# Performance work log

Measured on AMD Instinct MI355X. Metric: run time of the kernel, lower is better.

Reference implementation:

```python
import jax, jax.numpy as jnp
import numpy as np

B = 4096       # batch_size
D = 128        # projection dim
TEMP = 0.5     # temperature
EPS = 1e-12    # F.normalize eps


def setup_inputs() -> dict:
    key = jax.random.key(0)
    k1, k2 = jax.random.split(key)
    zi = jax.random.normal(k1, (B, D), dtype=jnp.float32)
    zj = jax.random.normal(k2, (B, D), dtype=jnp.float32)
    return {"zi": zi, "zj": zj}


def _l2_normalize(x):
    n = jnp.sqrt(jnp.sum(x * x, axis=-1, keepdims=True))
    return x / jnp.maximum(n, EPS)


def reference(zi, zj):
    zi_n = _l2_normalize(zi)
    zj_n = _l2_normalize(zj)

    # four [B, B] similarity matrices
    lii = jnp.matmul(zi_n, zi_n.T) / TEMP
    lij = jnp.matmul(zi_n, zj_n.T) / TEMP
    lji = jnp.matmul(zj_n, zi_n.T) / TEMP
    ljj = jnp.matmul(zj_n, zj_n.T) / TEMP

    # positives: diagonal of ij and ji (row-major gather of ~mask == diagonal)
    pos = jnp.concatenate([jnp.diagonal(lij), jnp.diagonal(lji)], axis=0)[:, None]  # [2B, 1]

    # off-diagonal gather: for row r, columns != r (preserves row-major order of mask gather)
    r = jnp.arange(B)[:, None]          # [B, 1]
    c = jnp.arange(B - 1)[None, :]      # [1, B-1]
    cols = c + (c >= r).astype(c.dtype)  # [B, B-1]

    def offdiag(m):
        return jnp.take_along_axis(m, cols, axis=1)  # [B, B-1]

    neg_i = jnp.concatenate([offdiag(lii), offdiag(lij)], axis=1)  # [B, 2B-2]
    neg_j = jnp.concatenate([offdiag(lji), offdiag(ljj)], axis=1)  # [B, 2B-2]
    neg = jnp.concatenate([neg_i, neg_j], axis=0)                  # [2B, 2B-2]

    logits = jnp.concatenate([pos, neg], axis=1)                   # [2B, 2B-1]

    # cross-entropy with all labels == 0
    loss = jnp.mean(jax.nn.logsumexp(logits, axis=1) - logits[:, 0])
    return loss
```

## Files before the change

kernel.cpp:

```cpp
#include <hip/hip_runtime.h>
#include <hip/hip_bf16.h>

#define BATCH   4096
#define TWO_B   8192
#define DIM     128
#define INV_TEMP 2.0f
#define EXP_SCALE (2.0f * 1.442695040888963f)

typedef __attribute__((ext_vector_type(8))) short bf16x8;
typedef __attribute__((ext_vector_type(4))) float f32x4;

#define CS 8
#define NPART (CS * 2)

#define ZB_BYTES   (TWO_B * DIM * 2)
#define RS_OFFSET  ZB_BYTES
#define PS_OFFSET  (RS_OFFSET + NPART * TWO_B * 4)

__global__ __launch_bounds__(256) void k_normalize(const float* __restrict__ zi,
                                                   const float* __restrict__ zj,
                                                   __hip_bfloat16* __restrict__ zb,
                                                   float* __restrict__ ps) {
    int w = threadIdx.x >> 6;
    int lane = threadIdx.x & 63;
    int r = blockIdx.x * 4 + w;

    float2 vi = *reinterpret_cast<const float2*>(zi + (size_t)r * DIM + lane * 2);
    float2 vj = *reinterpret_cast<const float2*>(zj + (size_t)r * DIM + lane * 2);
    float ssi = vi.x * vi.x + vi.y * vi.y;
    float ssj = vj.x * vj.x + vj.y * vj.y;
    #pragma unroll
    for (int m = 1; m < 64; m <<= 1) {
        ssi += __shfl_xor(ssi, m, 64);
        ssj += __shfl_xor(ssj, m, 64);
    }
    float invi = 1.0f / fmaxf(sqrtf(ssi), 1e-12f);
    float invj = 1.0f / fmaxf(sqrtf(ssj), 1e-12f);

    float nix = vi.x * invi, niy = vi.y * invi;
    float njx = vj.x * invj, njy = vj.y * invj;

    __hip_bfloat162 hi2, hj2;
    hi2.x = __float2bfloat16(nix);
    hi2.y = __float2bfloat16(niy);
    hj2.x = __float2bfloat16(njx);
    hj2.y = __float2bfloat16(njy);
    *reinterpret_cast<__hip_bfloat162*>(zb + (size_t)r * DIM + lane * 2) = hi2;
    *reinterpret_cast<__hip_bfloat162*>(zb + (size_t)(r + BATCH) * DIM + lane * 2) = hj2;

    float d = nix * njx + niy * njy;
    #pragma unroll
    for (int m = 1; m < 64; m <<= 1) d += __shfl_xor(d, m, 64);

    __shared__ float red[4];
    if (lane == 0) red[w] = d;
    __syncthreads();
    if (threadIdx.x == 0)
        ps[blockIdx.x] = red[0] + red[1] + red[2] + red[3];
}

__global__ __launch_bounds__(256) void k_sim(const __hip_bfloat16* __restrict__ zb,
                                             float* __restrict__ rs) {
    __shared__ unsigned short As[128 * 128];
    __shared__ unsigned short Bs[128 * 128];

    const int t = threadIdx.x;
    const int rowBlk = blockIdx.x / CS;
    const int split  = blockIdx.x % CS;
    const int rowBase = rowBlk * 128;

    #pragma unroll
    for (int it = 0; it < 8; ++it) {
        int chunk = t + it * 256;
        int row = chunk >> 4;
        int blk = chunk & 15;
        bf16x8 v = *reinterpret_cast<const bf16x8*>(zb + (size_t)(rowBase + row) * DIM + blk * 8);
        int sb = blk ^ (row & 7);
        *reinterpret_cast<bf16x8*>(reinterpret_cast<char*>(As) + row * 256 + sb * 16) = v;
    }

    const int w    = t >> 6;
    const int lane = t & 63;
    const int wr = w >> 1, wc = w & 1;
    const int lo = lane & 15, hi = lane >> 4;

    float psum[4][4];
    #pragma unroll
    for (int i = 0; i < 4; ++i)
        #pragma unroll
        for (int p = 0; p < 4; ++p) psum[i][p] = 0.0f;

    for (int ct = 0; ct < 8; ++ct) {
        const int colBase = split * 1024 + ct * 128;
        __syncthreads();
        #pragma unroll
        for (int it = 0; it < 8; ++it) {
            int chunk = t + it * 256;
            int row = chunk >> 4;
            int blk = chunk & 15;
            bf16x8 v = *reinterpret_cast<const bf16x8*>(zb + (size_t)(colBase + row) * DIM + blk * 8);
            int sb = blk ^ (row & 7);
            *reinterpret_cast<bf16x8*>(reinterpret_cast<char*>(Bs) + row * 256 + sb * 16) = v;
        }
        __syncthreads();

        f32x4 acc[4][4];
        #pragma unroll
        for (int i = 0; i < 4; ++i)
            #pragma unroll
            for (int j = 0; j < 4; ++j) acc[i][j] = (f32x4){0.f, 0.f, 0.f, 0.f};

        #pragma unroll
        for (int ks = 0; ks < 4; ++ks) {
            bf16x8 a[4], b[4];
            #pragma unroll
            for (int i = 0; i < 4; ++i) {
                int rA = wr * 64 + i * 16 + lo;
                int ba = (ks * 4 + hi) ^ (rA & 7);
                a[i] = *reinterpret_cast<const bf16x8*>(
                    reinterpret_cast<const char*>(As) + rA * 256 + ba * 16);
                int rB = wc * 64 + i * 16 + lo;
                int bb = (ks * 4 + hi) ^ (rB & 7);
                b[i] = *reinterpret_cast<const bf16x8*>(
                    reinterpret_cast<const char*>(Bs) + rB * 256 + bb * 16);
            }
            #pragma unroll
            for (int i = 0; i < 4; ++i)
                #pragma unroll
                for (int j = 0; j < 4; ++j)
                    acc[i][j] = __builtin_amdgcn_mfma_f32_16x16x32_bf16(a[i], b[j], acc[i][j], 0, 0, 0);
        }

        #pragma unroll
        for (int i = 0; i < 4; ++i) {
            int grBase = rowBase + wr * 64 + i * 16 + hi * 4;
            #pragma unroll
            for (int p = 0; p < 4; ++p) {
                int gr = grBase + p;
                float s = 0.0f;
                #pragma unroll
                for (int j = 0; j < 4; ++j) {
                    int gc = colBase + wc * 64 + j * 16 + lo;
                    float e = exp2f(acc[i][j][p] * EXP_SCALE);
                    s += (gr == gc) ? 0.0f : e;
                }
                psum[i][p] += s;
            }
        }
    }

    #pragma unroll
    for (int i = 0; i < 4; ++i) {
        #pragma unroll
        for (int p = 0; p < 4; ++p) {
            float s = psum[i][p];
            s += __shfl_xor(s, 1, 64);
            s += __shfl_xor(s, 2, 64);
            s += __shfl_xor(s, 4, 64);
            s += __shfl_xor(s, 8, 64);
            if (lo == 0)
                rs[(size_t)(split * 2 + wc) * TWO_B +
                   rowBase + wr * 64 + i * 16 + hi * 4 + p] = s;
        }
    }
}

__global__ __launch_bounds__(1024) void k_final(const float* __restrict__ rs,
                                                const float* __restrict__ ps,
                                                float* __restrict__ out) {
    __shared__ float redl[1024];
    __shared__ float redp[1024];
    const int t = threadIdx.x;

    float s = 0.0f;
    for (int r = t; r < TWO_B; r += 1024) {
        float acc = 0.0f;
        #pragma unroll
        for (int c = 0; c < NPART; ++c) acc += rs[(size_t)c * TWO_B + r];
        s += logf(acc);
    }
    float p = (t < 1024) ? ps[t] : 0.0f;

    redl[t] = s;
    redp[t] = p;
    __syncthreads();
    #pragma unroll
    for (int off = 512; off > 0; off >>= 1) {
        if (t < off) {
            redl[t] += redl[t + off];
            redp[t] += redp[t + off];
        }
        __syncthreads();
    }
    if (t == 0)
        out[0] = (redl[0] - 2.0f * INV_TEMP * redp[0]) / (float)TWO_B;
}

extern "C" void kernel_launch(void* const* d_in, const int* in_sizes, int n_in,
                              void* d_out, int out_size, void* d_ws, size_t ws_size,
                              hipStream_t stream) {
    const float* zi = (const float*)d_in[0];
    const float* zj = (const float*)d_in[1];
    float* out = (float*)d_out;

    char* ws = (char*)d_ws;
    __hip_bfloat16* zb = (__hip_bfloat16*)ws;
    float* rs = (float*)(ws + RS_OFFSET);
    float* ps = (float*)(ws + PS_OFFSET);

    k_normalize<<<BATCH / 4, 256, 0, stream>>>(zi, zj, zb, ps);
    k_sim<<<(TWO_B / 128) * CS, 256, 0, stream>>>(zb, rs);
    k_final<<<1, 1024, 0, stream>>>(rs, ps, out);
}
```

Before: 50.82 us.

## Drop LDS staging in similarity kernel, fold exp scale into bf16 inputs, atomic row sums

The similarity kernel no longer stages tiles in shared memory. Each wave keeps its own 64 rows of A in registers and loads B fragments for each 64-column tile straight from global memory, so block-wide barriers disappear. The exp2 scale is folded into the normalized bf16 vectors by multiplying by sqrt(2·log2e), which removes a multiply per element, and the diagonal mask is only applied on diagonal tiles. Partial row sums are combined with atomicAdd into a single buffer that the normalize kernel zeroes, which shrinks the final reduction. The trade-off is that waves no longer share B tiles, so cache and global load traffic goes up. Folding the scale before bf16 rounding also slightly changes precision.

```diff
diff --git a/kernel.cpp b/kernel.cpp
--- a/kernel.cpp
+++ b/kernel.cpp
@@ -5,25 +5,27 @@
 #define TWO_B   8192
 #define DIM     128
 #define INV_TEMP 2.0f
-#define EXP_SCALE (2.0f * 1.442695040888963f)
+#define SFOLD 1.6986436f
 
 typedef __attribute__((ext_vector_type(8))) short bf16x8;
 typedef __attribute__((ext_vector_type(4))) float f32x4;
 
-#define CS 8
-#define NPART (CS * 2)
+#define CS 16
 
 #define ZB_BYTES   (TWO_B * DIM * 2)
 #define RS_OFFSET  ZB_BYTES
-#define PS_OFFSET  (RS_OFFSET + NPART * TWO_B * 4)
+#define PS_OFFSET  (RS_OFFSET + TWO_B * 4)
 
 __global__ __launch_bounds__(256) void k_normalize(const float* __restrict__ zi,
                                                    const float* __restrict__ zj,
                                                    __hip_bfloat16* __restrict__ zb,
-                                                   float* __restrict__ ps) {
+                                                   float* __restrict__ ps,
+                                                   float* __restrict__ rowsum) {
     int w = threadIdx.x >> 6;
     int lane = threadIdx.x & 63;
     int r = blockIdx.x * 4 + w;
+
+    if (threadIdx.x < 8) rowsum[blockIdx.x * 8 + threadIdx.x] = 0.0f;
 
     float2 vi = *reinterpret_cast<const float2*>(zi + (size_t)r * DIM + lane * 2);
     float2 vj = *reinterpret_cast<const float2*>(zj + (size_t)r * DIM + lane * 2);
@@ -41,10 +43,10 @@
     float njx = vj.x * invj, njy = vj.y * invj;
 
     __hip_bfloat162 hi2, hj2;
-    hi2.x = __float2bfloat16(nix);
-    hi2.y = __float2bfloat16(niy);
-    hj2.x = __float2bfloat16(njx);
-    hj2.y = __float2bfloat16(njy);
+    hi2.x = __float2bfloat16(nix * SFOLD);
+    hi2.y = __float2bfloat16(niy * SFOLD);
+    hj2.x = __float2bfloat16(njx * SFOLD);
+    hj2.y = __float2bfloat16(njy * SFOLD);
     *reinterpret_cast<__hip_bfloat162*>(zb + (size_t)r * DIM + lane * 2) = hi2;
     *reinterpret_cast<__hip_bfloat162*>(zb + (size_t)(r + BATCH) * DIM + lane * 2) = hj2;
 
@@ -59,31 +61,28 @@
         ps[blockIdx.x] = red[0] + red[1] + red[2] + red[3];
 }
 
-__global__ __launch_bounds__(256) void k_sim(const __hip_bfloat16* __restrict__ zb,
-                                             float* __restrict__ rs) {
-    __shared__ unsigned short As[128 * 128];
-    __shared__ unsigned short Bs[128 * 128];
-
+__global__ __launch_bounds__(256, 2) void k_sim(const __hip_bfloat16* __restrict__ zb,
+                                                float* __restrict__ rowsum) {
     const int t = threadIdx.x;
-    const int rowBlk = blockIdx.x / CS;
-    const int split  = blockIdx.x % CS;
-    const int rowBase = rowBlk * 128;
-
-    #pragma unroll
-    for (int it = 0; it < 8; ++it) {
-        int chunk = t + it * 256;
-        int row = chunk >> 4;
-        int blk = chunk & 15;
-        bf16x8 v = *reinterpret_cast<const bf16x8*>(zb + (size_t)(rowBase + row) * DIM + blk * 8);
-        int sb = blk ^ (row & 7);
-        *reinterpret_cast<bf16x8*>(reinterpret_cast<char*>(As) + row * 256 + sb * 16) = v;
-    }
-
-    const int w    = t >> 6;
+    const int w = t >> 6;
     const int lane = t & 63;
-    const int wr = w >> 1, wc = w & 1;
     const int lo = lane & 15, hi = lane >> 4;
 
+    const int rowBlock = blockIdx.x / CS;
+    const int split    = blockIdx.x % CS;
+    const int rowBase  = rowBlock * 256 + w * 64;
+
+    const char* zbB = reinterpret_cast<const char*>(zb);
+
+    bf16x8 a[4][4];
+    #pragma unroll
+    for (int i = 0; i < 4; ++i) {
+        const char* rp = zbB + (size_t)(rowBase + i * 16 + lo) * 256 + hi * 16;
+        #pragma unroll
+        for (int ks = 0; ks < 4; ++ks)
+            a[i][ks] = *reinterpret_cast<const bf16x8*>(rp + ks * 64);
+    }
+
     float psum[4][4];
     #pragma unroll
     for (int i = 0; i < 4; ++i)
@@ -91,18 +90,16 @@
         for (int p = 0; p < 4; ++p) psum[i][p] = 0.0f;
 
     for (int ct = 0; ct < 8; ++ct) {
-        const int colBase = split * 1024 + ct * 128;
-        __syncthreads();
-        #pragma unroll
-        for (int it = 0; it < 8; ++it) {
-            int chunk = t + it * 256;
-            int row = chunk >> 4;
-            int blk = chunk & 15;
-            bf16x8 v = *reinterpret_cast<const bf16x8*>(zb + (size_t)(colBase + row) * DIM + blk * 8);
-            int sb = blk ^ (row & 7);
-            *reinterpret_cast<bf16x8*>(reinterpret_cast<char*>(Bs) + row * 256 + sb * 16) = v;
-        }
-        __syncthreads();
+        const int colBase = split * 512 + ct * 64;
+
+        bf16x8 b[4][4];
+        #pragma unroll
+        for (int j = 0; j < 4; ++j) {
+            const char* rp = zbB + (size_t)(colBase + j * 16 + lo) * 256 + hi * 16;
+            #pragma unroll
+            for (int ks = 0; ks < 4; ++ks)
+                b[j][ks] = *reinterpret_cast<const bf16x8*>(rp + ks * 64);
+        }
 
         f32x4 acc[4][4];
         #pragma unroll
@@ -111,41 +108,38 @@
             for (int j = 0; j < 4; ++j) acc[i][j] = (f32x4){0.f, 0.f, 0.f, 0.f};
 
         #pragma unroll
-        for (int ks = 0; ks < 4; ++ks) {
-            bf16x8 a[4], b[4];
-            #pragma unroll
-            for (int i = 0; i < 4; ++i) {
-                int rA = wr * 64 + i * 16 + lo;
-                int ba = (ks * 4 + hi) ^ (rA & 7);
-                a[i] = *reinterpret_cast<const bf16x8*>(
-                    reinterpret_cast<const char*>(As) + rA * 256 + ba * 16);
-                int rB = wc * 64 + i * 16 + lo;
-                int bb = (ks * 4 + hi) ^ (rB & 7);
-                b[i] = *reinterpret_cast<const bf16x8*>(
-                    reinterpret_cast<const char*>(Bs) + rB * 256 + bb * 16);
-            }
+        for (int ks = 0; ks < 4; ++ks)
             #pragma unroll
             for (int i = 0; i < 4; ++i)
                 #pragma unroll
                 for (int j = 0; j < 4; ++j)
-                    acc[i][j] = __builtin_amdgcn_mfma_f32_16x16x32_bf16(a[i], b[j], acc[i][j], 0, 0, 0);
-        }
-
-        #pragma unroll
-        for (int i = 0; i < 4; ++i) {
-            int grBase = rowBase + wr * 64 + i * 16 + hi * 4;
-            #pragma unroll
-            for (int p = 0; p < 4; ++p) {
-                int gr = grBase + p;
-                float s = 0.0f;
+                    acc[i][j] = __builtin_amdgcn_mfma_f32_16x16x32_bf16(
+                        a[i][ks], b[j][ks], acc[i][j], 0, 0, 0);
+
+        if (colBase == rowBase) {
+            #pragma unroll
+            for (int i = 0; i < 4; ++i)
                 #pragma unroll
-                for (int j = 0; j < 4; ++j) {
-                    int gc = colBase + wc * 64 + j * 16 + lo;
-                    float e = exp2f(acc[i][j][p] * EXP_SCALE);
-                    s += (gr == gc) ? 0.0f : e;
+                for (int p = 0; p < 4; ++p) {
+                    float s = 0.0f;
+                    #pragma unroll
+                    for (int j = 0; j < 4; ++j) {
+                        float e = exp2f(acc[i][j][p]);
+                        if (j == i && lo == hi * 4 + p) e = 0.0f;
+                        s += e;
+                    }
+                    psum[i][p] += s;
                 }
-                psum[i][p] += s;
-            }
+        } else {
+            #pragma unroll
+            for (int i = 0; i < 4; ++i)
+                #pragma unroll
+                for (int p = 0; p < 4; ++p) {
+                    float s = 0.0f;
+                    #pragma unroll
+                    for (int j = 0; j < 4; ++j) s += exp2f(acc[i][j][p]);
+                    psum[i][p] += s;
+                }
         }
     }
 
@@ -159,13 +153,12 @@
             s += __shfl_xor(s, 4, 64);
             s += __shfl_xor(s, 8, 64);
             if (lo == 0)
-                rs[(size_t)(split * 2 + wc) * TWO_B +
-                   rowBase + wr * 64 + i * 16 + hi * 4 + p] = s;
-        }
-    }
-}
-
-__global__ __launch_bounds__(1024) void k_final(const float* __restrict__ rs,
+                atomicAdd(&rowsum[rowBase + i * 16 + hi * 4 + p], s);
+        }
+    }
+}
+
+__global__ __launch_bounds__(1024) void k_final(const float* __restrict__ rowsum,
                                                 const float* __restrict__ ps,
                                                 float* __restrict__ out) {
     __shared__ float redl[1024];
@@ -173,13 +166,9 @@
     const int t = threadIdx.x;
 
     float s = 0.0f;
-    for (int r = t; r < TWO_B; r += 1024) {
-        float acc = 0.0f;
-        #pragma unroll
-        for (int c = 0; c < NPART; ++c) acc += rs[(size_t)c * TWO_B + r];
-        s += logf(acc);
-    }
-    float p = (t < 1024) ? ps[t] : 0.0f;
+    #pragma unroll
+    for (int q = 0; q < TWO_B / 1024; ++q) s += logf(rowsum[t + q * 1024]);
+    float p = ps[t];
 
     redl[t] = s;
     redp[t] = p;
@@ -205,10 +194,10 @@
 
     char* ws = (char*)d_ws;
     __hip_bfloat16* zb = (__hip_bfloat16*)ws;
-    float* rs = (float*)(ws + RS_OFFSET);
+    float* rowsum = (float*)(ws + RS_OFFSET);
     float* ps = (float*)(ws + PS_OFFSET);
 
-    k_normalize<<<BATCH / 4, 256, 0, stream>>>(zi, zj, zb, ps);
-    k_sim<<<(TWO_B / 128) * CS, 256, 0, stream>>>(zb, rs);
-    k_final<<<1, 1024, 0, stream>>>(rs, ps, out);
-}
+    k_normalize<<<BATCH / 4, 256, 0, stream>>>(zi, zj, zb, ps, rowsum);
+    k_sim<<<(TWO_B / 256) * CS, 256, 0, stream>>>(zb, rowsum);
+    k_final<<<1, 1024, 0, stream>>>(rowsum, ps, out);
+}
```

New measurement: 50.09 us. About the same (-1.4%).
